# Kernel optimization log

Measured on AMD Instinct MI355X. Metric: run time of the kernel, lower is better.

## Reference

```python
import jax, jax.numpy as jnp
import numpy as np

N_NODES = 50000
N_EDGES = 800000
NFEAT = 512
NHID = 128


def gcn_conv(x, W, b, src, dst, n_nodes):
    """PyG-style GCNConv: self-loops + symmetric deg^{-1/2} normalization."""
    # degrees over edges incl. self-loops (src/dst already contain them)
    deg = jax.ops.segment_sum(jnp.ones_like(src, dtype=x.dtype), dst,
                              num_segments=n_nodes)
    dinv = jnp.where(deg > 0, jax.lax.rsqrt(deg), 0.0)
    norm = dinv[src] * dinv[dst]            # [E+N]
    h = x @ W                               # [N, out] dense transform first (out <= in)
    msgs = h[src] * norm[:, None]           # gather + scale
    out = jax.ops.segment_sum(msgs, dst, num_segments=n_nodes)  # scatter-add
    return out + b


def setup_inputs() -> dict:
    key = jax.random.key(0)
    k1, k2, k3, k4 = jax.random.split(key, 4)
    x = jax.random.normal(k1, (N_NODES, NFEAT), dtype=jnp.float32)
    edge_index = jax.random.randint(k2, (2, N_EDGES), 0, N_NODES, dtype=jnp.int64)
    W1 = jax.random.normal(k3, (NFEAT, 2 * NHID), dtype=jnp.float32) / np.sqrt(NFEAT)
    b1 = jnp.zeros((2 * NHID,), dtype=jnp.float32)
    W2 = jax.random.normal(k4, (2 * NHID, NHID), dtype=jnp.float32) / np.sqrt(2 * NHID)
    b2 = jnp.zeros((NHID,), dtype=jnp.float32)
    return {"x": x, "edge_index": edge_index, "W1": W1, "b1": b1, "W2": W2, "b2": b2}


def reference(x, edge_index, W1, b1, W2, b2):
    n = x.shape[0]
    loop = jnp.arange(n, dtype=edge_index.dtype)
    src = jnp.concatenate([edge_index[0], loop])  # add self-loops once, reuse per layer
    dst = jnp.concatenate([edge_index[1], loop])
    h = jax.nn.relu(gcn_conv(x, W1, b1, src, dst, n))
    # dropout is identity in eval mode (reference runs in inference mode)
    out = gcn_conv(h, W2, b2, src, dst, n)
    return out
```

## Files before the change

kernel.cpp:

```cpp
#include <hip/hip_runtime.h>
#include <cstdint>
#include <cstddef>

#define NFEAT 512
#define NH1   256
#define NH2   128

#define SCAN_BLOCK 256
#define SCAN_ELEMS 4
#define SCAN_TILE  (SCAN_BLOCK * SCAN_ELEMS)

#define P_CHUNKS 128
#define HHALF    25088
#define NP       (2 * HHALF)

typedef __attribute__((ext_vector_type(8))) short short8;
typedef __attribute__((ext_vector_type(4))) float float4v;

__device__ __forceinline__ unsigned short f2bf(float f) {
    unsigned int u = __float_as_uint(f);
    u += 0x7fffu + ((u >> 16) & 1u);
    return (unsigned short)(u >> 16);
}
__device__ __forceinline__ float bf2f(unsigned short u) {
    return __uint_as_float(((unsigned int)u) << 16);
}

__device__ __forceinline__ void load_lds16(const void* g, void* l) {
    __builtin_amdgcn_global_load_lds(
        (const __attribute__((address_space(1))) void*)g,
        (__attribute__((address_space(3))) void*)l, 16, 0, 0);
}

__global__ __launch_bounds__(256) void k_hist(const int* __restrict__ dst,
                                              int* __restrict__ hist, int E, int CE) {
    __shared__ int lh[HHALF];
    const int c    = blockIdx.x >> 1;
    const int hf   = blockIdx.x & 1;
    const int base = hf * HHALF;
    for (int i = threadIdx.x; i < HHALF; i += 256) lh[i] = 0;
    __syncthreads();
    const int lo = c * CE;
    const int hi = lo + CE < E ? lo + CE : E;
    for (int e = lo + (int)threadIdx.x; e < hi; e += 256) {
        const int d = dst[e] - base;
        if ((unsigned)d < (unsigned)HHALF) atomicAdd(&lh[d], 1);
    }
    __syncthreads();
    int* outp = hist + (size_t)c * NP + base;
    for (int i = threadIdx.x; i < HHALF; i += 256) outp[i] = lh[i];
}

__global__ void k_colreduce(const int* __restrict__ hist, int* __restrict__ degi,
                            float* __restrict__ dinv, int N) {
    const int d = blockIdx.x * blockDim.x + threadIdx.x;
    if (d >= N) return;
    int s = 0;
#pragma unroll 8
    for (int c = 0; c < P_CHUNKS; ++c) s += hist[(size_t)c * NP + d];
    degi[d] = s;
    dinv[d] = rsqrtf((float)(s + 1));
}

__global__ void k_coloffs(int* __restrict__ hist, const int* __restrict__ row_start,
                          int N) {
    const int d = blockIdx.x * blockDim.x + threadIdx.x;
    if (d >= N) return;
    int run = row_start[d];
    for (int c = 0; c < P_CHUNKS; ++c) {
        int* p = &hist[(size_t)c * NP + d];
        const int t = *p;
        *p = run;
        run += t;
    }
}

__global__ __launch_bounds__(256) void k_place(const int* __restrict__ src,
                                               const int* __restrict__ dst,
                                               const int* __restrict__ hist,
                                               int* __restrict__ csr_src, int E, int CE) {
    __shared__ int lcur[HHALF];
    const int c    = blockIdx.x >> 1;
    const int hf   = blockIdx.x & 1;
    const int base = hf * HHALF;
    const int* offp = hist + (size_t)c * NP + base;
    for (int i = threadIdx.x; i < HHALF; i += 256) lcur[i] = offp[i];
    __syncthreads();
    const int lo = c * CE;
    const int hi = lo + CE < E ? lo + CE : E;
    for (int e = lo + (int)threadIdx.x; e < hi; e += 256) {
        const int d = dst[e] - base;
        if ((unsigned)d < (unsigned)HHALF) {
            const int p = atomicAdd(&lcur[d], 1);
            csr_src[p] = src[e];
        }
    }
}

__global__ __launch_bounds__(SCAN_BLOCK) void k_scan1(
    const int* __restrict__ degi, int* __restrict__ blocksums, int N) {
    __shared__ int red[SCAN_BLOCK];
    const int t = threadIdx.x;
    const int base = blockIdx.x * SCAN_TILE + t * SCAN_ELEMS;
    int s = 0;
#pragma unroll
    for (int i = 0; i < SCAN_ELEMS; ++i) {
        const int idx = base + i;
        if (idx < N) s += degi[idx];
    }
    red[t] = s;
    __syncthreads();
    for (int off = SCAN_BLOCK / 2; off > 0; off >>= 1) {
        if (t < off) red[t] += red[t + off];
        __syncthreads();
    }
    if (t == 0) blocksums[blockIdx.x] = red[0];
}

__global__ __launch_bounds__(1024) void k_scan2(
    const int* __restrict__ blocksums, int* __restrict__ blockoffs,
    int* __restrict__ row_start, int nb, int N) {
    __shared__ int sm[1024];
    const int t = threadIdx.x;
    const int v = (t < nb) ? blocksums[t] : 0;
    sm[t] = v;
    __syncthreads();
    for (int off = 1; off < 1024; off <<= 1) {
        const int x = (t >= off) ? sm[t - off] : 0;
        __syncthreads();
        sm[t] += x;
        __syncthreads();
    }
    if (t < nb) blockoffs[t] = sm[t] - v;
    if (t == 1023) row_start[N] = sm[1023];
}

__global__ __launch_bounds__(SCAN_BLOCK) void k_scan3(
    const int* __restrict__ degi, const int* __restrict__ blockoffs,
    int* __restrict__ row_start, int N) {
    __shared__ int tsum[SCAN_BLOCK];
    const int t = threadIdx.x;
    const int base = blockIdx.x * SCAN_TILE + t * SCAN_ELEMS;
    int v[SCAN_ELEMS];
    int s = 0;
#pragma unroll
    for (int i = 0; i < SCAN_ELEMS; ++i) {
        const int idx = base + i;
        v[i] = (idx < N) ? degi[idx] : 0;
        s += v[i];
    }
    tsum[t] = s;
    __syncthreads();
    for (int off = 1; off < SCAN_BLOCK; off <<= 1) {
        const int x = (t >= off) ? tsum[t - off] : 0;
        __syncthreads();
        tsum[t] += x;
        __syncthreads();
    }
    int excl = blockoffs[blockIdx.x] + tsum[t] - s;
#pragma unroll
    for (int i = 0; i < SCAN_ELEMS; ++i) {
        const int idx = base + i;
        if (idx < N) row_start[idx] = excl;
        excl += v[i];
    }
}

__global__ void k_cvt_w(const float* __restrict__ W1, unsigned short* __restrict__ W1t,
                        const float* __restrict__ W2, unsigned short* __restrict__ W2t) {
    const int i = blockIdx.x * blockDim.x + threadIdx.x;
    const int T1 = NFEAT * NH1;
    const int T2 = NH1 * NH2;
    if (i < T1) {
        const int k = i / NH1, n = i % NH1;
        W1t[(size_t)n * NFEAT + k] = f2bf(W1[i]);
    } else if (i < T1 + T2) {
        const int j = i - T1;
        const int k = j / NH2, n = j % NH2;
        W2t[(size_t)n * NH1 + k] = f2bf(W2[j]);
    }
}

__global__ __launch_bounds__(512) void gemm_x_fused(
    const float* __restrict__ x, const float* __restrict__ dinv,
    const unsigned short* __restrict__ Bt, unsigned short* __restrict__ C,
    int Nrows, int K) {
    __shared__ unsigned short As[128 * 32];
    __shared__ unsigned short Bs[256 * 32];
    const int t    = threadIdx.x;
    const int wave = t >> 6, lane = t & 63;
    const int row0 = blockIdx.x * 128;
    const int quad = lane >> 4, l15 = lane & 15;
    const int wm = (wave >> 2) * 64;
    const int wn = (wave & 3) * 64;

    const int arow = t >> 2;
    const int ak   = (t & 3) * 8;
    const int gr   = (row0 + arow < Nrows) ? row0 + arow : Nrows - 1;
    const float wd = dinv[gr];
    const float* gx = x + (size_t)gr * K + ak;
    unsigned short* lA = &As[arow * 32 + ak];

    const int brow = t >> 2;
    const int bk   = (t & 3) * 8;
    const unsigned short* gB0 = Bt + (size_t)brow * K + bk;
    const unsigned short* gB1 = Bt + (size_t)(128 + brow) * K + bk;
    unsigned short* lB0 = &Bs[wave * 512];
    unsigned short* lB1 = &Bs[128 * 32 + wave * 512];

    float4v acc[4][4] = {};

    for (int k0 = 0; k0 < K; k0 += 32) {
        __syncthreads();
        load_lds16(gB0 + k0, lB0);
        load_lds16(gB1 + k0, lB1);
        const float4 v0 = *(const float4*)(gx + k0);
        const float4 v1 = *(const float4*)(gx + k0 + 4);
        short8 o;
        o[0] = (short)f2bf(v0.x * wd); o[1] = (short)f2bf(v0.y * wd);
        o[2] = (short)f2bf(v0.z * wd); o[3] = (short)f2bf(v0.w * wd);
        o[4] = (short)f2bf(v1.x * wd); o[5] = (short)f2bf(v1.y * wd);
        o[6] = (short)f2bf(v1.z * wd); o[7] = (short)f2bf(v1.w * wd);
        *(short8*)lA = o;
        __syncthreads();

        short8 a[4], b[4];
#pragma unroll
        for (int i = 0; i < 4; ++i) {
            a[i] = *(const short8*)&As[(wm + i * 16 + l15) * 32 + quad * 8];
            b[i] = *(const short8*)&Bs[(wn + i * 16 + l15) * 32 + quad * 8];
        }
#pragma unroll
        for (int mt = 0; mt < 4; ++mt)
#pragma unroll
            for (int nt = 0; nt < 4; ++nt)
                acc[mt][nt] = __builtin_amdgcn_mfma_f32_16x16x32_bf16(
                    a[mt], b[nt], acc[mt][nt], 0, 0, 0);
    }

#pragma unroll
    for (int mt = 0; mt < 4; ++mt) {
#pragma unroll
        for (int nt = 0; nt < 4; ++nt) {
            const int c = wn + nt * 16 + l15;
#pragma unroll
            for (int r = 0; r < 4; ++r) {
                const int row = row0 + wm + mt * 16 + quad * 4 + r;
                C[(size_t)row * NH1 + c] = f2bf(acc[mt][nt][r]);
            }
        }
    }
}

__global__ __launch_bounds__(256) void gemm_bf16(
    const unsigned short* __restrict__ A, const unsigned short* __restrict__ Bt,
    unsigned short* __restrict__ C, int N, int K) {
    __shared__ unsigned short As[128 * 32];
    __shared__ unsigned short Bs[128 * 32];
    const int t    = threadIdx.x;
    const int wave = t >> 6, lane = t & 63;
    const int row0 = blockIdx.y * 128, col0 = blockIdx.x * 128;
    const int wm = (wave >> 1) * 64, wn = (wave & 1) * 64;
    const int sr = lane >> 2;
    const int sk = (lane & 3) * 8;
    const int quad = lane >> 4, l15 = lane & 15;

    const int ca = wave * 2;
    const unsigned short* gA0 = A  + (size_t)(row0 + ca * 16 + sr) * K + sk;
    const unsigned short* gA1 = gA0 + (size_t)16 * K;
    const unsigned short* gB0 = Bt + (size_t)(col0 + ca * 16 + sr) * K + sk;
    const unsigned short* gB1 = gB0 + (size_t)16 * K;
    unsigned short* lA0 = &As[ca * 512];
    unsigned short* lA1 = &As[(ca + 1) * 512];
    unsigned short* lB0 = &Bs[ca * 512];
    unsigned short* lB1 = &Bs[(ca + 1) * 512];

    float4v acc[4][4] = {};

    for (int k0 = 0; k0 < K; k0 += 32) {
        __syncthreads();
        load_lds16(gA0 + k0, lA0);
        load_lds16(gA1 + k0, lA1);
        load_lds16(gB0 + k0, lB0);
        load_lds16(gB1 + k0, lB1);
        __syncthreads();

        short8 a[4], b[4];
#pragma unroll
        for (int i = 0; i < 4; ++i) {
            a[i] = *(const short8*)&As[(wm + i * 16 + l15) * 32 + quad * 8];
            b[i] = *(const short8*)&Bs[(wn + i * 16 + l15) * 32 + quad * 8];
        }
#pragma unroll
        for (int mt = 0; mt < 4; ++mt)
#pragma unroll
            for (int nt = 0; nt < 4; ++nt)
                acc[mt][nt] = __builtin_amdgcn_mfma_f32_16x16x32_bf16(
                    a[mt], b[nt], acc[mt][nt], 0, 0, 0);
    }

#pragma unroll
    for (int mt = 0; mt < 4; ++mt) {
#pragma unroll
        for (int nt = 0; nt < 4; ++nt) {
            const int c = col0 + wn + nt * 16 + l15;
#pragma unroll
            for (int r = 0; r < 4; ++r) {
                const int row = row0 + wm + mt * 16 + quad * 4 + r;
                C[(size_t)row * N + c] = f2bf(acc[mt][nt][r]);
            }
        }
    }
}

template <int F, bool RELU, bool OUTF32>
__global__ __launch_bounds__(256) void k_gather(
    const int* __restrict__ row_start, const int* __restrict__ csr_src,
    const float* __restrict__ dinv, const unsigned short* __restrict__ h,
    const float* __restrict__ bias, unsigned short* __restrict__ ob,
    float* __restrict__ of, int N) {
    const int gid  = blockIdx.x * blockDim.x + threadIdx.x;
    const int node = gid >> 6;
    const int lane = gid & 63;
    if (node >= N) return;

    constexpr int EL = F / 64;
    const float wd = dinv[node];
    const int jb = row_start[node];
    const int je = row_start[node + 1];
    const unsigned short* hl = h + (size_t)lane * EL;

    float acc[EL];
    {
        const unsigned short* hp = hl + (size_t)node * F;
        if (EL == 4) {
            const ushort4 v = *(const ushort4*)hp;
            acc[0] = bf2f(v.x); acc[1] = bf2f(v.y);
            acc[2] = bf2f(v.z); acc[3] = bf2f(v.w);
        } else {
            const ushort2 v = *(const ushort2*)hp;
            acc[0] = bf2f(v.x); acc[1] = bf2f(v.y);
        }
    }

    for (int j0 = jb; j0 < je; j0 += 64) {
        int jj = j0 + lane;
        if (jj >= je) jj = je - 1;
        const int myi = csr_src[jj];
        const int rem = je - j0;
        const int cnt = rem < 64 ? rem : 64;
        int i = 0;
        for (; i + 4 <= cnt; i += 4) {
            const int s0 = __shfl(myi, i + 0);
            const int s1 = __shfl(myi, i + 1);
            const int s2 = __shfl(myi, i + 2);
            const int s3 = __shfl(myi, i + 3);
            if (EL == 4) {
                const ushort4 v0 = *(const ushort4*)(hl + (size_t)s0 * F);
                const ushort4 v1 = *(const ushort4*)(hl + (size_t)s1 * F);
                const ushort4 v2 = *(const ushort4*)(hl + (size_t)s2 * F);
                const ushort4 v3 = *(const ushort4*)(hl + (size_t)s3 * F);
                acc[0] += bf2f(v0.x) + bf2f(v1.x) + bf2f(v2.x) + bf2f(v3.x);
                acc[1] += bf2f(v0.y) + bf2f(v1.y) + bf2f(v2.y) + bf2f(v3.y);
                acc[2] += bf2f(v0.z) + bf2f(v1.z) + bf2f(v2.z) + bf2f(v3.z);
                acc[3] += bf2f(v0.w) + bf2f(v1.w) + bf2f(v2.w) + bf2f(v3.w);
            } else {
                const ushort2 v0 = *(const ushort2*)(hl + (size_t)s0 * F);
                const ushort2 v1 = *(const ushort2*)(hl + (size_t)s1 * F);
                const ushort2 v2 = *(const ushort2*)(hl + (size_t)s2 * F);
                const ushort2 v3 = *(const ushort2*)(hl + (size_t)s3 * F);
                acc[0] += bf2f(v0.x) + bf2f(v1.x) + bf2f(v2.x) + bf2f(v3.x);
                acc[1] += bf2f(v0.y) + bf2f(v1.y) + bf2f(v2.y) + bf2f(v3.y);
            }
        }
        for (; i < cnt; ++i) {
            const int s = __shfl(myi, i);
            const unsigned short* hp = hl + (size_t)s * F;
            if (EL == 4) {
                const ushort4 v = *(const ushort4*)hp;
                acc[0] += bf2f(v.x); acc[1] += bf2f(v.y);
                acc[2] += bf2f(v.z); acc[3] += bf2f(v.w);
            } else {
                const ushort2 v = *(const ushort2*)hp;
                acc[0] += bf2f(v.x); acc[1] += bf2f(v.y);
            }
        }
    }

#pragma unroll
    for (int i = 0; i < EL; ++i) {
        float v = fmaf(acc[i], wd, bias[lane * EL + i]);
        if (OUTF32) {
            of[(size_t)node * F + lane * EL + i] = v;
        } else {
            if (RELU) v = fmaxf(v, 0.f);
            ob[(size_t)node * F + lane * EL + i] = f2bf(v * wd);
        }
    }
}

extern "C" void kernel_launch(void* const* d_in, const int* in_sizes, int n_in,
                              void* d_out, int out_size, void* d_ws, size_t ws_size,
                              hipStream_t stream) {
    const float* x   = (const float*)d_in[0];
    const int*   ei  = (const int*)d_in[1];
    const float* W1  = (const float*)d_in[2];
    const float* b1  = (const float*)d_in[3];
    const float* W2  = (const float*)d_in[4];
    const float* b2  = (const float*)d_in[5];
    float*       out = (float*)d_out;

    const int N = in_sizes[0] / NFEAT;
    const int E = in_sizes[1] / 2;
    const int Mp = ((N + 127) / 128) * 128;
    const int* srcp = ei;
    const int* dstp = ei + E;
    const int nScanBlocks = (N + SCAN_TILE - 1) / SCAN_TILE;
    const int CE = (E + P_CHUNKS - 1) / P_CHUNKS;

    char* wsb = (char*)d_ws;
    auto take = [&](size_t bytes) {
        char* p = wsb;
        wsb += (bytes + 255) & ~(size_t)255;
        return p;
    };
    int*   degi      = (int*)take((size_t)N * 4);
    int*   row_start = (int*)take((size_t)(N + 1) * 4);
    int*   csr_src   = (int*)take((size_t)E * 4);
    int*   blocksums = (int*)take((size_t)1024 * 4);
    int*   blockoffs = (int*)take((size_t)1024 * 4);
    float* dinv      = (float*)take((size_t)N * 4);
    unsigned short* h2r = (unsigned short*)take((size_t)Mp * NFEAT * 2);
    unsigned short* W1t = (unsigned short*)take((size_t)NH1 * NFEAT * 2);
    unsigned short* W2t = (unsigned short*)take((size_t)NH2 * NH1 * 2);
    const size_t hBytes    = (size_t)Mp * NH1 * 2;
    const size_t histBytes = (size_t)P_CHUNKS * NP * 4;
    char* big = take(histBytes > 2 * hBytes ? histBytes : 2 * hBytes);
    int*            hist = (int*)big;
    unsigned short* h    = (unsigned short*)big;
    unsigned short* h1   = (unsigned short*)(big + hBytes);
    unsigned short* h2   = h2r;

    k_hist<<<P_CHUNKS * 2, 256, 0, stream>>>(dstp, hist, E, CE);
    k_colreduce<<<(N + 255) / 256, 256, 0, stream>>>(hist, degi, dinv, N);
    k_scan1<<<nScanBlocks, SCAN_BLOCK, 0, stream>>>(degi, blocksums, N);
    k_scan2<<<1, 1024, 0, stream>>>(blocksums, blockoffs, row_start, nScanBlocks, N);
    k_scan3<<<nScanBlocks, SCAN_BLOCK, 0, stream>>>(degi, blockoffs, row_start, N);
    k_coloffs<<<(N + 255) / 256, 256, 0, stream>>>(hist, row_start, N);
    k_place<<<P_CHUNKS * 2, 256, 0, stream>>>(srcp, dstp, hist, csr_src, E, CE);

    {
        const int total = NFEAT * NH1 + NH1 * NH2;
        k_cvt_w<<<(total + 255) / 256, 256, 0, stream>>>(W1, W1t, W2, W2t);
    }

    gemm_x_fused<<<Mp / 128, 512, 0, stream>>>(x, dinv, W1t, h, N, NFEAT);
    {
        int total = N * 64;
        k_gather<NH1, true, false><<<(total + 255) / 256, 256, 0, stream>>>(
            row_start, csr_src, dinv, h, b1, h1, nullptr, N);
    }

    {
        dim3 g(NH2 / 128, Mp / 128);
        gemm_bf16<<<g, 256, 0, stream>>>(h1, W2t, h2, NH2, NH1);
    }
    {
        int total = N * 64;
        k_gather<NH2, false, true><<<(total + 255) / 256, 256, 0, stream>>>(
            row_start, csr_src, dinv, h2, b2, nullptr, out, N);
    }
}
```

Baseline: 346.7 us.

## Replace chunked histogram CSR build with global atomic degree count and placement

Removes the per-chunk shared-memory histograms, the column-reduce and column-offset passes, and builds the CSR with global atomics instead: one pass counts degrees and a second pass places edges by bumping row_start as a cursor. The weight conversion is fused into the degree kernel, and dinv is computed inside the first scan kernel. Because placement advances row_start to each row's end, the gather now reads row ranges as [row_start[node-1], row_start[node]). This cuts several launches and the large histogram traffic, in exchange for contended global atomics and a nondeterministic edge order within each row.

```diff
diff --git a/kernel.cpp b/kernel.cpp
--- a/kernel.cpp
+++ b/kernel.cpp
@@ -9,10 +9,6 @@
 #define SCAN_BLOCK 256
 #define SCAN_ELEMS 4
 #define SCAN_TILE  (SCAN_BLOCK * SCAN_ELEMS)
-
-#define P_CHUNKS 128
-#define HHALF    25088
-#define NP       (2 * HHALF)
 
 typedef __attribute__((ext_vector_type(8))) short short8;
 typedef __attribute__((ext_vector_type(4))) float float4v;
@@ -32,73 +28,33 @@
         (__attribute__((address_space(3))) void*)l, 16, 0, 0);
 }
 
-__global__ __launch_bounds__(256) void k_hist(const int* __restrict__ dst,
-                                              int* __restrict__ hist, int E, int CE) {
-    __shared__ int lh[HHALF];
-    const int c    = blockIdx.x >> 1;
-    const int hf   = blockIdx.x & 1;
-    const int base = hf * HHALF;
-    for (int i = threadIdx.x; i < HHALF; i += 256) lh[i] = 0;
-    __syncthreads();
-    const int lo = c * CE;
-    const int hi = lo + CE < E ? lo + CE : E;
-    for (int e = lo + (int)threadIdx.x; e < hi; e += 256) {
-        const int d = dst[e] - base;
-        if ((unsigned)d < (unsigned)HHALF) atomicAdd(&lh[d], 1);
-    }
-    __syncthreads();
-    int* outp = hist + (size_t)c * NP + base;
-    for (int i = threadIdx.x; i < HHALF; i += 256) outp[i] = lh[i];
-}
-
-__global__ void k_colreduce(const int* __restrict__ hist, int* __restrict__ degi,
-                            float* __restrict__ dinv, int N) {
-    const int d = blockIdx.x * blockDim.x + threadIdx.x;
-    if (d >= N) return;
-    int s = 0;
-#pragma unroll 8
-    for (int c = 0; c < P_CHUNKS; ++c) s += hist[(size_t)c * NP + d];
-    degi[d] = s;
-    dinv[d] = rsqrtf((float)(s + 1));
-}
-
-__global__ void k_coloffs(int* __restrict__ hist, const int* __restrict__ row_start,
-                          int N) {
-    const int d = blockIdx.x * blockDim.x + threadIdx.x;
-    if (d >= N) return;
-    int run = row_start[d];
-    for (int c = 0; c < P_CHUNKS; ++c) {
-        int* p = &hist[(size_t)c * NP + d];
-        const int t = *p;
-        *p = run;
-        run += t;
-    }
-}
-
-__global__ __launch_bounds__(256) void k_place(const int* __restrict__ src,
-                                               const int* __restrict__ dst,
-                                               const int* __restrict__ hist,
-                                               int* __restrict__ csr_src, int E, int CE) {
-    __shared__ int lcur[HHALF];
-    const int c    = blockIdx.x >> 1;
-    const int hf   = blockIdx.x & 1;
-    const int base = hf * HHALF;
-    const int* offp = hist + (size_t)c * NP + base;
-    for (int i = threadIdx.x; i < HHALF; i += 256) lcur[i] = offp[i];
-    __syncthreads();
-    const int lo = c * CE;
-    const int hi = lo + CE < E ? lo + CE : E;
-    for (int e = lo + (int)threadIdx.x; e < hi; e += 256) {
-        const int d = dst[e] - base;
-        if ((unsigned)d < (unsigned)HHALF) {
-            const int p = atomicAdd(&lcur[d], 1);
-            csr_src[p] = src[e];
+__global__ __launch_bounds__(256) void k_deg_cvtw(
+    const int* __restrict__ dst, int* __restrict__ degi,
+    const float* __restrict__ W1, unsigned short* __restrict__ W1t,
+    const float* __restrict__ W2, unsigned short* __restrict__ W2t,
+    int E, int degBlocks) {
+    const int b = blockIdx.x;
+    if (b < degBlocks) {
+        const int e = b * 256 + (int)threadIdx.x;
+        if (e < E) atomicAdd(&degi[dst[e]], 1);
+    } else {
+        const int i = (b - degBlocks) * 256 + (int)threadIdx.x;
+        const int T1 = NFEAT * NH1;
+        const int T2 = NH1 * NH2;
+        if (i < T1) {
+            const int k = i / NH1, n = i % NH1;
+            W1t[(size_t)n * NFEAT + k] = f2bf(W1[i]);
+        } else if (i < T1 + T2) {
+            const int j = i - T1;
+            const int k = j / NH2, n = j % NH2;
+            W2t[(size_t)n * NH1 + k] = f2bf(W2[j]);
         }
     }
 }
 
 __global__ __launch_bounds__(SCAN_BLOCK) void k_scan1(
-    const int* __restrict__ degi, int* __restrict__ blocksums, int N) {
+    const int* __restrict__ degi, int* __restrict__ blocksums,
+    float* __restrict__ dinv, int N) {
     __shared__ int red[SCAN_BLOCK];
     const int t = threadIdx.x;
     const int base = blockIdx.x * SCAN_TILE + t * SCAN_ELEMS;
@@ -106,7 +62,11 @@
 #pragma unroll
     for (int i = 0; i < SCAN_ELEMS; ++i) {
         const int idx = base + i;
-        if (idx < N) s += degi[idx];
+        if (idx < N) {
+            const int dg = degi[idx];
+            s += dg;
+            dinv[idx] = rsqrtf((float)(dg + 1));
+        }
     }
     red[t] = s;
     __syncthreads();
@@ -166,18 +126,15 @@
     }
 }
 
-__global__ void k_cvt_w(const float* __restrict__ W1, unsigned short* __restrict__ W1t,
-                        const float* __restrict__ W2, unsigned short* __restrict__ W2t) {
-    const int i = blockIdx.x * blockDim.x + threadIdx.x;
-    const int T1 = NFEAT * NH1;
-    const int T2 = NH1 * NH2;
-    if (i < T1) {
-        const int k = i / NH1, n = i % NH1;
-        W1t[(size_t)n * NFEAT + k] = f2bf(W1[i]);
-    } else if (i < T1 + T2) {
-        const int j = i - T1;
-        const int k = j / NH2, n = j % NH2;
-        W2t[(size_t)n * NH1 + k] = f2bf(W2[j]);
+__global__ __launch_bounds__(256) void k_place2(
+    const int* __restrict__ src, const int* __restrict__ dst,
+    int* __restrict__ cursor ,
+    int* __restrict__ csr_src, int E) {
+    const int e = blockIdx.x * 256 + (int)threadIdx.x;
+    if (e < E) {
+        const int d = dst[e];
+        const int p = atomicAdd(&cursor[d], 1);
+        csr_src[p] = src[e];
     }
 }
 
@@ -326,8 +283,8 @@
 
     constexpr int EL = F / 64;
     const float wd = dinv[node];
-    const int jb = row_start[node];
-    const int je = row_start[node + 1];
+    const int je = row_start[node];
+    const int jb = (node == 0) ? 0 : row_start[node - 1];
     const unsigned short* hl = h + (size_t)lane * EL;
 
     float acc[EL];
@@ -416,7 +373,6 @@
     const int* srcp = ei;
     const int* dstp = ei + E;
     const int nScanBlocks = (N + SCAN_TILE - 1) / SCAN_TILE;
-    const int CE = (E + P_CHUNKS - 1) / P_CHUNKS;
 
     char* wsb = (char*)d_ws;
     auto take = [&](size_t bytes) {
@@ -430,29 +386,26 @@
     int*   blocksums = (int*)take((size_t)1024 * 4);
     int*   blockoffs = (int*)take((size_t)1024 * 4);
     float* dinv      = (float*)take((size_t)N * 4);
-    unsigned short* h2r = (unsigned short*)take((size_t)Mp * NFEAT * 2);
+    unsigned short* h2r = (unsigned short*)take((size_t)Mp * NH2 * 2);
     unsigned short* W1t = (unsigned short*)take((size_t)NH1 * NFEAT * 2);
     unsigned short* W2t = (unsigned short*)take((size_t)NH2 * NH1 * 2);
-    const size_t hBytes    = (size_t)Mp * NH1 * 2;
-    const size_t histBytes = (size_t)P_CHUNKS * NP * 4;
-    char* big = take(histBytes > 2 * hBytes ? histBytes : 2 * hBytes);
-    int*            hist = (int*)big;
+    const size_t hBytes = (size_t)Mp * NH1 * 2;
+    char* big = take(2 * hBytes);
     unsigned short* h    = (unsigned short*)big;
     unsigned short* h1   = (unsigned short*)(big + hBytes);
     unsigned short* h2   = h2r;
 
-    k_hist<<<P_CHUNKS * 2, 256, 0, stream>>>(dstp, hist, E, CE);
-    k_colreduce<<<(N + 255) / 256, 256, 0, stream>>>(hist, degi, dinv, N);
-    k_scan1<<<nScanBlocks, SCAN_BLOCK, 0, stream>>>(degi, blocksums, N);
+    hipMemsetAsync(degi, 0, (size_t)N * 4, stream);
+    {
+        const int degBlocks = (E + 255) / 256;
+        const int cvtBlocks = (NFEAT * NH1 + NH1 * NH2 + 255) / 256;
+        k_deg_cvtw<<<degBlocks + cvtBlocks, 256, 0, stream>>>(
+            dstp, degi, W1, W1t, W2, W2t, E, degBlocks);
+    }
+    k_scan1<<<nScanBlocks, SCAN_BLOCK, 0, stream>>>(degi, blocksums, dinv, N);
     k_scan2<<<1, 1024, 0, stream>>>(blocksums, blockoffs, row_start, nScanBlocks, N);
     k_scan3<<<nScanBlocks, SCAN_BLOCK, 0, stream>>>(degi, blockoffs, row_start, N);
-    k_coloffs<<<(N + 255) / 256, 256, 0, stream>>>(hist, row_start, N);
-    k_place<<<P_CHUNKS * 2, 256, 0, stream>>>(srcp, dstp, hist, csr_src, E, CE);
-
-    {
-        const int total = NFEAT * NH1 + NH1 * NH2;
-        k_cvt_w<<<(total + 255) / 256, 256, 0, stream>>>(W1, W1t, W2, W2t);
-    }
+    k_place2<<<(E + 255) / 256, 256, 0, stream>>>(srcp, dstp, row_start, csr_src, E);
 
     gemm_x_fused<<<Mp / 128, 512, 0, stream>>>(x, dinv, W1t, h, N, NFEAT);
     {
```

Measured after the change: 369.8 us. 6.7% more time.
